# Performance work log

Measured on AMD Instinct MI355X. Metric: run time of the kernel, lower is better.

Reference implementation:

```python
import jax, jax.numpy as jnp
import numpy as np

N_NODES = 100000
N_EDGES = 1600000
DIM = 64


def setup_inputs() -> dict:
    key = jax.random.key(0)
    k1, k2, k3 = jax.random.split(key, 3)
    x = jax.random.normal(k1, (N_NODES, DIM), dtype=jnp.float32)
    edge_index = jax.random.randint(k2, (2, N_EDGES), 0, N_NODES, dtype=jnp.int64)
    W = jax.random.normal(k3, (DIM, DIM), dtype=jnp.float32) * (1.0 / np.sqrt(DIM))
    b = jnp.zeros((DIM,), dtype=jnp.float32)
    return {"x": x, "edge_index": edge_index, "W": W, "b": b}


def reference(x, edge_index, W, b):
    # GCNConv (PyG defaults): add self-loops, symmetric normalization,
    # linear transform, scatter-add aggregation, bias; then ReLU.
    N = x.shape[0]
    loop = jnp.arange(N, dtype=edge_index.dtype)
    row = jnp.concatenate([edge_index[0], loop])  # source nodes
    col = jnp.concatenate([edge_index[1], loop])  # target nodes
    ew = jnp.ones(row.shape[0], dtype=x.dtype)

    deg = jax.ops.segment_sum(ew, col, num_segments=N)  # [N]
    dinv = jnp.where(deg > 0, jax.lax.rsqrt(deg), 0.0)
    norm = dinv[row] * ew * dinv[col]  # [E+N]

    xw = x @ W.T  # [N, D] small GEMM
    msg = norm[:, None] * xw[row]  # gather + scale, [E+N, D]
    out = jax.ops.segment_sum(msg, col, num_segments=N) + b  # scatter-add
    return jax.nn.relu(out)
```

## Files before the change

### kernel.cpp

```cpp
#include <hip/hip_runtime.h>
#include <hip/hip_bf16.h>

#define N_NODES 100000
#define N_EDGES 1600000
#define DIM 64
#define NBUCK 782
#define BK_NODES 128
#define CAP 2560
#define HA_EPB 16384
#define HA_BLOCKS 98

typedef unsigned int uint32;
typedef __attribute__((ext_vector_type(8))) short bf16x8;
typedef __attribute__((ext_vector_type(4))) float f32x4;

__device__ __forceinline__ float bflo(uint32 u) { return __uint_as_float(u << 16); }
__device__ __forceinline__ float bfhi(uint32 u) { return __uint_as_float(u & 0xffff0000u); }

__device__ __forceinline__ short f2bf(float f) {
    __hip_bfloat16 h = __float2bfloat16(f);
    return (short)__builtin_bit_cast(unsigned short, h);
}
__device__ __forceinline__ uint32 pack2bf(float lo, float hi) {
    unsigned short a = __builtin_bit_cast(unsigned short, __float2bfloat16(lo));
    unsigned short b = __builtin_bit_cast(unsigned short, __float2bfloat16(hi));
    return ((uint32)b << 16) | (uint32)a;
}

__global__ __launch_bounds__(1024) void zero_kernel(int* __restrict__ bcnt) {
    if (threadIdx.x < NBUCK) bcnt[threadIdx.x] = 0;
}

__global__ __launch_bounds__(1024) void scatter_kernel(const int* __restrict__ row,
                                                       const int* __restrict__ col,
                                                       int* __restrict__ bcnt,
                                                       int* __restrict__ pairs) {
    __shared__ int h[NBUCK];
    __shared__ int base[NBUCK];
    for (int i = threadIdx.x; i < NBUCK; i += 1024) h[i] = 0;
    __syncthreads();

    const int bstart = blockIdx.x * HA_EPB;
    int r[16], c[16];
#pragma unroll 16
    for (int k = 0; k < 16; ++k) {
        int e = bstart + threadIdx.x + k * 1024;
        if (e < N_EDGES) {
            r[k] = row[e];
            c[k] = col[e];
            atomicAdd(&h[c[k] >> 7], 1);
        }
    }
    __syncthreads();
    for (int i = threadIdx.x; i < NBUCK; i += 1024) {
        int v = h[i];
        base[i] = v ? atomicAdd(&bcnt[i], v) : 0;
        h[i] = 0;
    }
    __syncthreads();
#pragma unroll 16
    for (int k = 0; k < 16; ++k) {
        int e = bstart + threadIdx.x + k * 1024;
        if (e < N_EDGES) {
            int bk = c[k] >> 7;
            int pos = base[bk] + atomicAdd(&h[bk], 1);
            if (pos < CAP) pairs[bk * CAP + pos] = (r[k] << 7) | (c[k] & 127);
        }
    }
}

__global__ __launch_bounds__(256) void sort_kernel(const int* __restrict__ bcnt,
                                                   int* __restrict__ pairs,
                                                   int* __restrict__ info,
                                                   float* __restrict__ dinv) {
    __shared__ int cnt[BK_NODES];
    __shared__ int sc[BK_NODES];
    __shared__ int cur[BK_NODES];
    __shared__ int buf[CAP];
    const int b = blockIdx.x;
    const int tid = threadIdx.x;
    const int n = bcnt[b];
    if (tid < BK_NODES) cnt[tid] = 0;
    __syncthreads();
    for (int p = tid; p < n; p += 256) {
        int pk = pairs[b * CAP + p];
        buf[p] = pk;
        atomicAdd(&cnt[pk & 127], 1);
    }
    __syncthreads();
    if (tid < BK_NODES) sc[tid] = cnt[tid];
    __syncthreads();
    for (int off = 1; off < BK_NODES; off <<= 1) {
        int t = (tid < BK_NODES && tid >= off) ? sc[tid - off] : 0;
        __syncthreads();
        if (tid < BK_NODES) sc[tid] += t;
        __syncthreads();
    }
    if (tid < BK_NODES) {
        int ex = sc[tid] - cnt[tid];
        cur[tid] = ex;
        int node = b * BK_NODES + tid;
        if (node < N_NODES) {
            info[node] = ((b * CAP + ex) << 8) | cnt[tid];
            dinv[node] = rsqrtf((float)(cnt[tid] + 1));
        }
    }
    __syncthreads();
    for (int p = tid; p < n; p += 256) {
        int pk = buf[p];
        int pos = atomicAdd(&cur[pk & 127], 1);
        pairs[b * CAP + pos] = pk >> 7;
    }
}

__global__ __launch_bounds__(256) void gemm_kernel(const float* __restrict__ x,
                                                   const float* __restrict__ W,
                                                   const float* __restrict__ dinv,
                                                   uint32* __restrict__ sbw) {
    __shared__ float lds[64 * 64];
    const int wave = threadIdx.x >> 6;
    const int lane = threadIdx.x & 63;
    const int base = blockIdx.x * 64;
    const int r16 = lane & 15;
    const int kb = lane >> 4;

    bf16x8 wb[4][2];
#pragma unroll
    for (int t = 0; t < 4; ++t) {
#pragma unroll
        for (int h = 0; h < 2; ++h) {
            const float* wp = &W[(r16 + 16 * t) * DIM + 32 * h + kb * 8];
            float4 p0 = *(const float4*)wp;
            float4 p1 = *(const float4*)(wp + 4);
            bf16x8 f;
            f[0] = f2bf(p0.x); f[1] = f2bf(p0.y); f[2] = f2bf(p0.z); f[3] = f2bf(p0.w);
            f[4] = f2bf(p1.x); f[5] = f2bf(p1.y); f[6] = f2bf(p1.z); f[7] = f2bf(p1.w);
            wb[t][h] = f;
        }
    }

    int arow = base + wave * 16 + r16;
    if (arow >= N_NODES) arow = N_NODES - 1;
    bf16x8 af[2];
#pragma unroll
    for (int h = 0; h < 2; ++h) {
        const float* xp = &x[(size_t)arow * DIM + 32 * h + kb * 8];
        float4 p0 = *(const float4*)xp;
        float4 p1 = *(const float4*)(xp + 4);
        bf16x8 f;
        f[0] = f2bf(p0.x); f[1] = f2bf(p0.y); f[2] = f2bf(p0.z); f[3] = f2bf(p0.w);
        f[4] = f2bf(p1.x); f[5] = f2bf(p1.y); f[6] = f2bf(p1.z); f[7] = f2bf(p1.w);
        af[h] = f;
    }

    float dv[4];
#pragma unroll
    for (int i = 0; i < 4; ++i) {
        int rr = base + wave * 16 + kb * 4 + i;
        dv[i] = dinv[rr < N_NODES ? rr : N_NODES - 1];
    }

#pragma unroll
    for (int t = 0; t < 4; ++t) {
        f32x4 c = {0.0f, 0.0f, 0.0f, 0.0f};
        c = __builtin_amdgcn_mfma_f32_16x16x32_bf16(af[0], wb[t][0], c, 0, 0, 0);
        c = __builtin_amdgcn_mfma_f32_16x16x32_bf16(af[1], wb[t][1], c, 0, 0, 0);
#pragma unroll
        for (int i = 0; i < 4; ++i)
            lds[(wave * 16 + kb * 4 + i) * 64 + r16 + 16 * t] = c[i] * dv[i];
    }
    __syncthreads();

    int r = threadIdx.x >> 2;
    int cb = threadIdx.x & 3;
    int nrow = base + r;
    if (nrow < N_NODES) {
        const float* src = &lds[r * 64 + cb * 16];
        uint32 o[8];
#pragma unroll
        for (int j = 0; j < 8; ++j) {
            float2 f = *(const float2*)&src[2 * j];
            o[j] = pack2bf(f.x, f.y);
        }
        uint32* dst = sbw + (size_t)nrow * 32 + cb * 8;
        *(uint4*)dst = make_uint4(o[0], o[1], o[2], o[3]);
        *(uint4*)(dst + 4) = make_uint4(o[4], o[5], o[6], o[7]);
    }
}

__global__ __launch_bounds__(256) void agg_kernel(const int* __restrict__ info,
                                                  const int* __restrict__ srow,
                                                  const uint2* __restrict__ s4,
                                                  const float* __restrict__ dinv,
                                                  const float* __restrict__ bias,
                                                  float* __restrict__ out) {
    const int wid = blockIdx.x * 4 + (threadIdx.x >> 6);
    const int lane = threadIdx.x & 63;
    const int qn = lane >> 4;
    const int l = lane & 15;

    int n = wid * 4 + qn;
    const bool nvalid = n < N_NODES;
    const int nn = nvalid ? n : N_NODES - 1;
    const int iv = info[nn];
    const int start = iv >> 8;
    const int end = start + (iv & 255);

    float a0 = 0.0f, a1 = 0.0f, a2 = 0.0f, a3 = 0.0f;
    int p = start;
    for (; p + 3 < end; p += 4) {
        int r0 = srow[p], r1 = srow[p + 1], r2 = srow[p + 2], r3 = srow[p + 3];
        uint2 u0 = s4[(size_t)r0 * 16 + l];
        uint2 u1 = s4[(size_t)r1 * 16 + l];
        uint2 u2 = s4[(size_t)r2 * 16 + l];
        uint2 u3 = s4[(size_t)r3 * 16 + l];
        a0 += bflo(u0.x); a1 += bfhi(u0.x); a2 += bflo(u0.y); a3 += bfhi(u0.y);
        a0 += bflo(u1.x); a1 += bfhi(u1.x); a2 += bflo(u1.y); a3 += bfhi(u1.y);
        a0 += bflo(u2.x); a1 += bfhi(u2.x); a2 += bflo(u2.y); a3 += bfhi(u2.y);
        a0 += bflo(u3.x); a1 += bfhi(u3.x); a2 += bflo(u3.y); a3 += bfhi(u3.y);
    }
    int rem = end - p;
    if (rem > 0) {
        int i1 = (rem > 1) ? p + 1 : 0;
        int i2 = (rem > 2) ? p + 2 : 0;
        float m1 = (rem > 1) ? 1.0f : 0.0f;
        float m2 = (rem > 2) ? 1.0f : 0.0f;
        int r0 = srow[p], r1 = srow[i1], r2 = srow[i2];
        uint2 u0 = s4[(size_t)r0 * 16 + l];
        uint2 u1 = s4[(size_t)r1 * 16 + l];
        uint2 u2 = s4[(size_t)r2 * 16 + l];
        a0 += bflo(u0.x); a1 += bfhi(u0.x); a2 += bflo(u0.y); a3 += bfhi(u0.y);
        a0 = fmaf(m1, bflo(u1.x), a0); a1 = fmaf(m1, bfhi(u1.x), a1);
        a2 = fmaf(m1, bflo(u1.y), a2); a3 = fmaf(m1, bfhi(u1.y), a3);
        a0 = fmaf(m2, bflo(u2.x), a0); a1 = fmaf(m2, bfhi(u2.x), a1);
        a2 = fmaf(m2, bflo(u2.y), a2); a3 = fmaf(m2, bfhi(u2.y), a3);
    }

    if (nvalid) {
        uint2 us = s4[(size_t)n * 16 + l];
        a0 += bflo(us.x); a1 += bfhi(us.x); a2 += bflo(us.y); a3 += bfhi(us.y);
        float4 bb = *(const float4*)&bias[4 * l];
        float d = dinv[n];
        float4 o;
        o.x = fmaxf(fmaf(d, a0, bb.x), 0.0f);
        o.y = fmaxf(fmaf(d, a1, bb.y), 0.0f);
        o.z = fmaxf(fmaf(d, a2, bb.z), 0.0f);
        o.w = fmaxf(fmaf(d, a3, bb.w), 0.0f);
        *(float4*)&out[(size_t)n * DIM + 4 * l] = o;
    }
}

extern "C" void kernel_launch(void* const* d_in, const int* in_sizes, int n_in,
                              void* d_out, int out_size, void* d_ws, size_t ws_size,
                              hipStream_t stream) {
    const float* x    = (const float*)d_in[0];
    const int*   ei   = (const int*)d_in[1];
    const float* W    = (const float*)d_in[2];
    const float* bias = (const float*)d_in[3];
    float*       out  = (float*)d_out;

    const int* row = ei;
    const int* col = ei + N_EDGES;

    char* ws = (char*)d_ws;
    int*    bcnt  = (int*)(ws + 0);
    int*    info  = (int*)(ws + 4096);
    float*  dinv  = (float*)(ws + 404224);
    int*    pairs = (int*)(ws + 804352);
    uint32* sbw   = (uint32*)(ws + 8812160);

    zero_kernel<<<1, 1024, 0, stream>>>(bcnt);
    scatter_kernel<<<HA_BLOCKS, 1024, 0, stream>>>(row, col, bcnt, pairs);
    sort_kernel<<<NBUCK, 256, 0, stream>>>(bcnt, pairs, info, dinv);
    gemm_kernel<<<(N_NODES + 63) / 64, 256, 0, stream>>>(x, W, dinv, sbw);
    agg_kernel<<<(N_NODES + 15) / 16, 256, 0, stream>>>(info, pairs, (const uint2*)sbw,
                                                        dinv, bias, out);
}
```

Measured before the change: 94.57 us.

## Assign one wavefront per node in aggregation, shrink scatter blocks, use shuffle scan

The aggregation kernel now gives each node a full 64-lane wavefront instead of a quarter wavefront. Four 16-lane groups stride over the node's edges and are combined with cross-lane xor shuffles, which gives more memory-level parallelism per node and less load imbalance across high-degree nodes. The launch grows to four times as many blocks. The scatter kernel processes 4096 edges per block across 391 blocks instead of 16384 across 98, which spreads the histogram work over more CUs at the cost of more global atomics on bucket counters. The sort kernel's prefix scan switches from a shared-memory scan with many barriers to a wavefront shuffle scan.

```diff
diff --git a/kernel.cpp b/kernel.cpp
--- a/kernel.cpp
+++ b/kernel.cpp
@@ -7,8 +7,8 @@
 #define NBUCK 782
 #define BK_NODES 128
 #define CAP 2560
-#define HA_EPB 16384
-#define HA_BLOCKS 98
+#define HA_EPB 4096
+#define HA_BLOCKS 391
 
 typedef unsigned int uint32;
 typedef __attribute__((ext_vector_type(8))) short bf16x8;
@@ -37,13 +37,13 @@
                                                        int* __restrict__ pairs) {
     __shared__ int h[NBUCK];
     __shared__ int base[NBUCK];
-    for (int i = threadIdx.x; i < NBUCK; i += 1024) h[i] = 0;
+    if (threadIdx.x < NBUCK) h[threadIdx.x] = 0;
     __syncthreads();
 
     const int bstart = blockIdx.x * HA_EPB;
-    int r[16], c[16];
-#pragma unroll 16
-    for (int k = 0; k < 16; ++k) {
+    int r[4], c[4];
+#pragma unroll 4
+    for (int k = 0; k < 4; ++k) {
         int e = bstart + threadIdx.x + k * 1024;
         if (e < N_EDGES) {
             r[k] = row[e];
@@ -52,14 +52,14 @@
         }
     }
     __syncthreads();
-    for (int i = threadIdx.x; i < NBUCK; i += 1024) {
-        int v = h[i];
-        base[i] = v ? atomicAdd(&bcnt[i], v) : 0;
-        h[i] = 0;
-    }
-    __syncthreads();
-#pragma unroll 16
-    for (int k = 0; k < 16; ++k) {
+    if (threadIdx.x < NBUCK) {
+        int v = h[threadIdx.x];
+        base[threadIdx.x] = v ? atomicAdd(&bcnt[threadIdx.x], v) : 0;
+        h[threadIdx.x] = 0;
+    }
+    __syncthreads();
+#pragma unroll 4
+    for (int k = 0; k < 4; ++k) {
         int e = bstart + threadIdx.x + k * 1024;
         if (e < N_EDGES) {
             int bk = c[k] >> 7;
@@ -88,14 +88,19 @@
         atomicAdd(&cnt[pk & 127], 1);
     }
     __syncthreads();
-    if (tid < BK_NODES) sc[tid] = cnt[tid];
-    __syncthreads();
-    for (int off = 1; off < BK_NODES; off <<= 1) {
-        int t = (tid < BK_NODES && tid >= off) ? sc[tid - off] : 0;
-        __syncthreads();
-        if (tid < BK_NODES) sc[tid] += t;
-        __syncthreads();
-    }
+    if (tid < BK_NODES) {
+        int lane = tid & 63;
+        int sum = cnt[tid];
+#pragma unroll
+        for (int d = 1; d < 64; d <<= 1) {
+            int t = __shfl_up(sum, d);
+            if (lane >= d) sum += t;
+        }
+        sc[tid] = sum;
+    }
+    __syncthreads();
+    if (tid >= 64 && tid < BK_NODES) sc[tid] += sc[63];
+    __syncthreads();
     if (tid < BK_NODES) {
         int ex = sc[tid] - cnt[tid];
         cur[tid] = ex;
@@ -194,22 +199,23 @@
                                                   const float* __restrict__ dinv,
                                                   const float* __restrict__ bias,
                                                   float* __restrict__ out) {
-    const int wid = blockIdx.x * 4 + (threadIdx.x >> 6);
+    int n = __builtin_amdgcn_readfirstlane(blockIdx.x * 4 + (threadIdx.x >> 6));
+    if (n >= N_NODES) return;
     const int lane = threadIdx.x & 63;
-    const int qn = lane >> 4;
+    const int q = lane >> 4;
     const int l = lane & 15;
 
-    int n = wid * 4 + qn;
-    const bool nvalid = n < N_NODES;
-    const int nn = nvalid ? n : N_NODES - 1;
-    const int iv = info[nn];
+    const int iv = info[n];
     const int start = iv >> 8;
     const int end = start + (iv & 255);
 
     float a0 = 0.0f, a1 = 0.0f, a2 = 0.0f, a3 = 0.0f;
-    int p = start;
-    for (; p + 3 < end; p += 4) {
-        int r0 = srow[p], r1 = srow[p + 1], r2 = srow[p + 2], r3 = srow[p + 3];
+    int p = start + q;
+    for (; p + 12 < end; p += 16) {
+        int r0 = srow[p];
+        int r1 = srow[p + 4];
+        int r2 = srow[p + 8];
+        int r3 = srow[p + 12];
         uint2 u0 = s4[(size_t)r0 * 16 + l];
         uint2 u1 = s4[(size_t)r1 * 16 + l];
         uint2 u2 = s4[(size_t)r2 * 16 + l];
@@ -219,24 +225,18 @@
         a0 += bflo(u2.x); a1 += bfhi(u2.x); a2 += bflo(u2.y); a3 += bfhi(u2.y);
         a0 += bflo(u3.x); a1 += bfhi(u3.x); a2 += bflo(u3.y); a3 += bfhi(u3.y);
     }
-    int rem = end - p;
-    if (rem > 0) {
-        int i1 = (rem > 1) ? p + 1 : 0;
-        int i2 = (rem > 2) ? p + 2 : 0;
-        float m1 = (rem > 1) ? 1.0f : 0.0f;
-        float m2 = (rem > 2) ? 1.0f : 0.0f;
-        int r0 = srow[p], r1 = srow[i1], r2 = srow[i2];
+    for (; p < end; p += 4) {
+        int r0 = srow[p];
         uint2 u0 = s4[(size_t)r0 * 16 + l];
-        uint2 u1 = s4[(size_t)r1 * 16 + l];
-        uint2 u2 = s4[(size_t)r2 * 16 + l];
         a0 += bflo(u0.x); a1 += bfhi(u0.x); a2 += bflo(u0.y); a3 += bfhi(u0.y);
-        a0 = fmaf(m1, bflo(u1.x), a0); a1 = fmaf(m1, bfhi(u1.x), a1);
-        a2 = fmaf(m1, bflo(u1.y), a2); a3 = fmaf(m1, bfhi(u1.y), a3);
-        a0 = fmaf(m2, bflo(u2.x), a0); a1 = fmaf(m2, bfhi(u2.x), a1);
-        a2 = fmaf(m2, bflo(u2.y), a2); a3 = fmaf(m2, bfhi(u2.y), a3);
-    }
-
-    if (nvalid) {
+    }
+
+    a0 += __shfl_xor(a0, 16); a1 += __shfl_xor(a1, 16);
+    a2 += __shfl_xor(a2, 16); a3 += __shfl_xor(a3, 16);
+    a0 += __shfl_xor(a0, 32); a1 += __shfl_xor(a1, 32);
+    a2 += __shfl_xor(a2, 32); a3 += __shfl_xor(a3, 32);
+
+    if (lane < 16) {
         uint2 us = s4[(size_t)n * 16 + l];
         a0 += bflo(us.x); a1 += bfhi(us.x); a2 += bflo(us.y); a3 += bfhi(us.y);
         float4 bb = *(const float4*)&bias[4 * l];
@@ -273,6 +273,6 @@
     scatter_kernel<<<HA_BLOCKS, 1024, 0, stream>>>(row, col, bcnt, pairs);
     sort_kernel<<<NBUCK, 256, 0, stream>>>(bcnt, pairs, info, dinv);
     gemm_kernel<<<(N_NODES + 63) / 64, 256, 0, stream>>>(x, W, dinv, sbw);
-    agg_kernel<<<(N_NODES + 15) / 16, 256, 0, stream>>>(info, pairs, (const uint2*)sbw,
-                                                        dinv, bias, out);
-}
+    agg_kernel<<<(N_NODES + 3) / 4, 256, 0, stream>>>(info, pairs, (const uint2*)sbw,
+                                                      dinv, bias, out);
+}
```

New measurement: 107.3 us. 1.13x slower.
